# Kernel tuning notes

Measured on AMD Instinct MI355X. Metric: run time of the kernel, lower is better.

Reference implementation:

```python
import jax, jax.numpy as jnp
import numpy as np

EPS = 1e-5
C = 64  # in_channels == feat_channels == out_channels


def _ln(x, g, b):
    m = jnp.mean(x, axis=-1, keepdims=True)
    v = jnp.mean(jnp.square(x - m), axis=-1, keepdims=True)
    return (x - m) * jax.lax.rsqrt(v + EPS) * g + b


def setup_inputs() -> dict:
    key = jax.random.key(0)
    ks = jax.random.split(key, 10)
    bs, nc, H, W = 8, 80, 256, 256
    d = {
        "feat": jax.random.normal(ks[0], (bs, C, H, W), jnp.float32),
        "head": jax.random.normal(ks[1], (bs, nc, C, 1), jnp.float32),
        "pred": jax.random.normal(ks[2], (bs, nc, H // 2, W // 2), jnp.float32),
        # linear transforms (stored [in, out], applied as x @ W + b)
        "W_pred_t": jax.random.normal(ks[3], (C, 2 * C), jnp.float32) * 0.05,
        "b_pred_t": jnp.zeros((2 * C,), jnp.float32),
        "W_head_t": jax.random.normal(ks[4], (C, 2 * C), jnp.float32) * 0.05,
        "b_head_t": jnp.zeros((2 * C,), jnp.float32),
        "W_pred_g": jax.random.normal(ks[5], (C, C), jnp.float32) * 0.05,
        "b_pred_g": jnp.zeros((C,), jnp.float32),
        "W_head_g": jax.random.normal(ks[6], (C, C), jnp.float32) * 0.05,
        "b_head_g": jnp.zeros((C,), jnp.float32),
        "W_fc": jax.random.normal(ks[7], (C, C), jnp.float32) * 0.05,
        "b_fc": jnp.zeros((C,), jnp.float32),
        # layernorm params
        "g_pin": jnp.ones((C,), jnp.float32), "be_pin": jnp.zeros((C,), jnp.float32),
        "g_hin": jnp.ones((C,), jnp.float32), "be_hin": jnp.zeros((C,), jnp.float32),
        "g_pout": jnp.ones((C,), jnp.float32), "be_pout": jnp.zeros((C,), jnp.float32),
        "g_hout": jnp.ones((C,), jnp.float32), "be_hout": jnp.zeros((C,), jnp.float32),
        "g_fc": jnp.ones((C,), jnp.float32), "be_fc": jnp.zeros((C,), jnp.float32),
    }
    return d


def reference(feat, head, pred,
              W_pred_t, b_pred_t, W_head_t, b_head_t,
              W_pred_g, b_pred_g, W_head_g, b_head_g,
              W_fc, b_fc,
              g_pin, be_pin, g_hin, be_hin,
              g_pout, be_pout, g_hout, be_hout,
              g_fc, be_fc):
    bs, nc = head.shape[:2]
    H, W = feat.shape[2], feat.shape[3]
    pred_up = jax.image.resize(pred, (bs, nc, H, W), method="bilinear")
    pred_up = jax.nn.sigmoid(pred_up)
    # head-aware feature assembly: [bs, nc, C]
    assemble = jnp.einsum("bnhw,bchw->bnc", pred_up, feat)
    a = assemble.reshape(-1, C)                      # [BN, C]
    BN = a.shape[0]
    # head: [bs, nc, C, kk] -> [BN, kk, C]
    hd = jnp.transpose(head.reshape(bs, nc, C, -1), (0, 1, 3, 2)).reshape(BN, -1, C)

    pf = a @ W_pred_t + b_pred_t                     # [BN, 2C]
    pf_in, pf_out = pf[:, :C], pf[:, C:]
    hf = hd @ W_head_t + b_head_t                    # [BN, kk, 2C]
    hf_in, hf_out = hf[..., :C], hf[..., C:]

    gate = hf_in * pf_in[:, None, :]                 # [BN, kk, C]
    head_gate = jax.nn.sigmoid(_ln(gate @ W_head_g + b_head_g, g_hin, be_hin))
    pred_gate = jax.nn.sigmoid(_ln(gate @ W_pred_g + b_pred_g, g_pin, be_pin))

    hf_out = _ln(hf_out, g_hout, be_hout)
    pf_out = _ln(pf_out, g_pout, be_pout)

    upd = pred_gate * pf_out[:, None, :] + head_gate * hf_out
    upd = jax.nn.relu(_ln(upd @ W_fc + b_fc, g_fc, be_fc))
    upd = upd.reshape(bs, nc, -1, C)
    upd = jnp.transpose(upd, (0, 1, 3, 2)).reshape(bs, nc, C, 1, 1)
    return upd
```

## Files before the change

### kernel.cpp

```cpp
#include <hip/hip_runtime.h>
#include <hip/hip_bf16.h>


using bf16x8 = __attribute__((ext_vector_type(8))) short;
using f32x4  = __attribute__((ext_vector_type(4))) float;

#define NPART 64

__device__ __forceinline__ unsigned pk2(float lo, float hi) {
  union { __hip_bfloat162 h2; unsigned u; } cv;
  cv.h2 = __float22bfloat162_rn(make_float2(lo, hi));
  return cv.u;
}
__device__ __forceinline__ float sigAB(float a, float b) {
  return __builtin_amdgcn_rcpf(1.0f + __builtin_amdgcn_exp2f(-0.36067376f * a - 1.08202128f * b));
}
__device__ __forceinline__ float sigBA(float a, float b) {
  return __builtin_amdgcn_rcpf(1.0f + __builtin_amdgcn_exp2f(-1.08202128f * a - 0.36067376f * b));
}

__global__ __launch_bounds__(256, 2) void k_assemble(
    const float* __restrict__ feat, const float* __restrict__ pred,
    float* __restrict__ partial) {
  __shared__ __align__(16) unsigned short Pfrag[40 * 64 * 8];

  const int tid = threadIdx.x;
  const int b  = blockIdx.x >> 6;
  const int rb = blockIdx.x & 63;
  const int wid = tid >> 6, l = tid & 63;
  const int ch16 = l & 15, kg = l >> 4;
  const int c0 = wid << 4;
  const int h0 = rb * 4;
  const int gg = tid & 31, nb = tid >> 5;

  f32x4 acc[5] = {};

  const float* fwave = feat + (((size_t)(b * 64 + c0 + ch16)) << 16);
  const float* pbat  = pred + (((size_t)(b * 80)) << 14);

  float4 p0[10], p1[10];

  {
    const int j = h0 >> 1;
    const int r0 = (j > 0) ? j - 1 : 0, r1 = j;
    #pragma unroll
    for (int i = 0; i < 10; ++i) {
      const int n = nb + 8 * i;
      const float* pb = pbat + (((size_t)n) << 14);
      p0[i] = *(const float4*)(pb + (r0 << 7) + gg * 4);
      p1[i] = *(const float4*)(pb + (r1 << 7) + gg * 4);
    }
  }

  #pragma unroll
  for (int r = 0; r < 4; ++r) {
    const int h = h0 + r;
    const float wy0 = (r & 1) ? 0.75f : 0.25f;
    const float wy1 = (r & 1) ? 0.25f : 0.75f;

    #pragma unroll
    for (int i = 0; i < 10; ++i) {
      const int n = nb + 8 * i;
      const float y0 = wy0 * p0[i].x + wy1 * p1[i].x;
      const float y1 = wy0 * p0[i].y + wy1 * p1[i].y;
      const float y2 = wy0 * p0[i].z + wy1 * p1[i].z;
      const float y3 = wy0 * p0[i].w + wy1 * p1[i].w;
      float yl = __shfl_up(y3, 1, 64);   if (gg == 0)  yl = y0;
      float yr = __shfl_down(y0, 1, 64); if (gg == 31) yr = y3;
      float P[8];
      P[0] = sigAB(yl, y0); P[1] = sigBA(y0, y1);
      P[2] = sigAB(y0, y1); P[3] = sigBA(y1, y2);
      P[4] = sigAB(y1, y2); P[5] = sigBA(y2, y3);
      P[6] = sigAB(y2, y3); P[7] = sigBA(y3, yr);
      uint4 s;
      s.x = pk2(P[0], P[1]); s.y = pk2(P[2], P[3]);
      s.z = pk2(P[4], P[5]); s.w = pk2(P[6], P[7]);
      const int ks = gg >> 2, kgw = gg & 3;
      const int slot = kgw * 16 + ((n & 15) ^ ks);
      *(uint4*)&Pfrag[(((ks * 5 + (n >> 4)) * 64) + slot) * 8] = s;
    }
    __syncthreads();

    const float* fb = fwave + h * 256;
    float4 f[16];
    #pragma unroll
    for (int ks = 0; ks < 8; ++ks) {
      const int pw = ks * 32 + kg * 8;
      f[2 * ks]     = *(const float4*)(fb + pw);
      f[2 * ks + 1] = *(const float4*)(fb + pw + 4);
    }
    if (r < 3) {
      const int hn = h + 1;
      const int j = hn >> 1;
      int r0, r1;
      if ((hn & 1) == 0) { r0 = (j > 0) ? j - 1 : 0; r1 = j; }
      else               { r0 = j; r1 = (j < 127) ? j + 1 : 127; }
      #pragma unroll
      for (int i = 0; i < 10; ++i) {
        const int n = nb + 8 * i;
        const float* pb = pbat + (((size_t)n) << 14);
        p0[i] = *(const float4*)(pb + (r0 << 7) + gg * 4);
        p1[i] = *(const float4*)(pb + (r1 << 7) + gg * 4);
      }
    }
    #pragma unroll
    for (int ks = 0; ks < 8; ++ks) {
      const float4 f0 = f[2 * ks], f1 = f[2 * ks + 1];
      union { uint4 u; bf16x8 v; } bu;
      bu.u.x = pk2(f0.x, f0.y); bu.u.y = pk2(f0.z, f0.w);
      bu.u.z = pk2(f1.x, f1.y); bu.u.w = pk2(f1.z, f1.w);
      const int slot = kg * 16 + (ch16 ^ ks);
      #pragma unroll
      for (int m = 0; m < 5; ++m) {
        const bf16x8 af = *(const bf16x8*)&Pfrag[(((ks * 5 + m) * 64) + slot) * 8];
        acc[m] = __builtin_amdgcn_mfma_f32_16x16x32_bf16(af, bu.v, acc[m], 0, 0, 0);
      }
    }
    __syncthreads();
  }

  float* po = partial + ((size_t)(b * NPART + rb)) * (80 * 64);
  #pragma unroll
  for (int m = 0; m < 5; ++m) {
    #pragma unroll
    for (int q = 0; q < 4; ++q) {
      const int n = m * 16 + kg * 4 + q;
      po[n * 64 + c0 + ch16] = acc[m][q];
    }
  }
}

__device__ __forceinline__ float wred64(float v) {
  #pragma unroll
  for (int off = 32; off > 0; off >>= 1) v += __shfl_xor(v, off, 64);
  return v;
}
__device__ __forceinline__ float lnorm(float x, const float* __restrict__ g,
                                       const float* __restrict__ be, int l) {
  const float m = wred64(x) * 0.015625f;
  const float d = x - m;
  const float var = wred64(d * d) * 0.015625f;
  return d * rsqrtf(var + 1e-5f) * g[l] + be[l];
}
__device__ __forceinline__ float sigmf(float x) {
  return __builtin_amdgcn_rcpf(1.0f + __builtin_amdgcn_exp2f(-1.44269504f * x));
}

__global__ __launch_bounds__(256) void k_head(
    const float* __restrict__ partial, const float* __restrict__ head,
    const float* __restrict__ Wpt, const float* __restrict__ bpt,
    const float* __restrict__ Wht, const float* __restrict__ bht,
    const float* __restrict__ Wpg, const float* __restrict__ bpg,
    const float* __restrict__ Whg, const float* __restrict__ bhg,
    const float* __restrict__ Wfc, const float* __restrict__ bfc,
    const float* __restrict__ g_pin, const float* __restrict__ be_pin,
    const float* __restrict__ g_hin, const float* __restrict__ be_hin,
    const float* __restrict__ g_pout, const float* __restrict__ be_pout,
    const float* __restrict__ g_hout, const float* __restrict__ be_hout,
    const float* __restrict__ g_fc, const float* __restrict__ be_fc,
    float* __restrict__ out) {
  __shared__ float rows[4][4][64];
  const int tid = threadIdx.x, wid = tid >> 6, l = tid & 63;
  const int r = blockIdx.x * 4 + wid;
  const int b = r / 80, n = r % 80;

  const float* pp = partial + (size_t)b * (NPART * 80 * 64) + n * 64 + l;
  float a_c = 0.f;
  #pragma unroll 8
  for (int jj = 0; jj < NPART; ++jj) a_c += pp[(size_t)jj * (80 * 64)];
  rows[wid][0][l] = a_c;
  rows[wid][1][l] = head[(size_t)r * 64 + l];
  __syncthreads();

  float pf_in = bpt[l], pf_out = bpt[64 + l];
  float hf_in = bht[l], hf_out = bht[64 + l];
  #pragma unroll 8
  for (int c = 0; c < 64; ++c) {
    const float av = rows[wid][0][c];
    const float hv = rows[wid][1][c];
    pf_in  += av * Wpt[c * 128 + l];
    pf_out += av * Wpt[c * 128 + 64 + l];
    hf_in  += hv * Wht[c * 128 + l];
    hf_out += hv * Wht[c * 128 + 64 + l];
  }
  const float gate = hf_in * pf_in;
  rows[wid][2][l] = gate;
  __syncthreads();

  float hg = bhg[l], pg = bpg[l];
  #pragma unroll 8
  for (int c = 0; c < 64; ++c) {
    const float gv = rows[wid][2][c];
    hg += gv * Whg[c * 64 + l];
    pg += gv * Wpg[c * 64 + l];
  }
  const float head_gate = sigmf(lnorm(hg, g_hin, be_hin, l));
  const float pred_gate = sigmf(lnorm(pg, g_pin, be_pin, l));
  const float hfo = lnorm(hf_out, g_hout, be_hout, l);
  const float pfo = lnorm(pf_out, g_pout, be_pout, l);
  const float upd = pred_gate * pfo + head_gate * hfo;
  rows[wid][3][l] = upd;
  __syncthreads();

  float fc = bfc[l];
  #pragma unroll 8
  for (int c = 0; c < 64; ++c)
    fc += rows[wid][3][c] * Wfc[c * 64 + l];
  float o = lnorm(fc, g_fc, be_fc, l);
  o = fmaxf(o, 0.f);
  out[(size_t)r * 64 + l] = o;
}

extern "C" void kernel_launch(void* const* d_in, const int* in_sizes, int n_in,
                              void* d_out, int out_size, void* d_ws, size_t ws_size,
                              hipStream_t stream) {
  const float* feat   = (const float*)d_in[0];
  const float* head   = (const float*)d_in[1];
  const float* pred   = (const float*)d_in[2];
  const float* Wpt    = (const float*)d_in[3];
  const float* bpt    = (const float*)d_in[4];
  const float* Wht    = (const float*)d_in[5];
  const float* bht    = (const float*)d_in[6];
  const float* Wpg    = (const float*)d_in[7];
  const float* bpg    = (const float*)d_in[8];
  const float* Whg    = (const float*)d_in[9];
  const float* bhg    = (const float*)d_in[10];
  const float* Wfc    = (const float*)d_in[11];
  const float* bfc    = (const float*)d_in[12];
  const float* g_pin  = (const float*)d_in[13];
  const float* be_pin = (const float*)d_in[14];
  const float* g_hin  = (const float*)d_in[15];
  const float* be_hin = (const float*)d_in[16];
  const float* g_pout = (const float*)d_in[17];
  const float* be_pout= (const float*)d_in[18];
  const float* g_hout = (const float*)d_in[19];
  const float* be_hout= (const float*)d_in[20];
  const float* g_fc   = (const float*)d_in[21];
  const float* be_fc  = (const float*)d_in[22];
  float* out = (float*)d_out;
  float* partial = (float*)d_ws;

  hipLaunchKernelGGL(k_assemble, dim3(8 * NPART), dim3(256), 0, stream,
                     feat, pred, partial);
  hipLaunchKernelGGL(k_head, dim3(160), dim3(256), 0, stream,
                     partial, head, Wpt, bpt, Wht, bht, Wpg, bpg, Whg, bhg,
                     Wfc, bfc, g_pin, be_pin, g_hin, be_hin, g_pout, be_pout,
                     g_hout, be_hout, g_fc, be_fc, out);
}
```

Before: 64.28 us.

## Split assemble into more row blocks and parallelize head partial reduction

The assemble kernel is templated on rows per block. When the workspace is large enough it launches 1024 blocks of 2 rows instead of 512 blocks of 4, and the launch bound rises to 3 blocks per CU. The software prefetch of the next pred rows is removed: each iteration now loads its pred and feat rows up front, and __syncthreads is replaced by a raw LDS waitcnt plus s_barrier. The head kernel switches to one block per row, with four waves splitting the partial-sum reduction and a single wave doing the MLP. This aims for more parallelism and occupancy, at the cost of a larger partial buffer and lost load/compute overlap.

```diff
diff --git a/kernel.cpp b/kernel.cpp
--- a/kernel.cpp
+++ b/kernel.cpp
@@ -4,8 +4,6 @@
 
 using bf16x8 = __attribute__((ext_vector_type(8))) short;
 using f32x4  = __attribute__((ext_vector_type(4))) float;
-
-#define NPART 64
 
 __device__ __forceinline__ unsigned pk2(float lo, float hi) {
   union { __hip_bfloat162 h2; unsigned u; } cv;
@@ -19,52 +17,58 @@
   return __builtin_amdgcn_rcpf(1.0f + __builtin_amdgcn_exp2f(-1.08202128f * a - 0.36067376f * b));
 }
 
-__global__ __launch_bounds__(256, 2) void k_assemble(
+template<int ROWS>
+__global__ __launch_bounds__(256, 3) void k_assemble(
     const float* __restrict__ feat, const float* __restrict__ pred,
     float* __restrict__ partial) {
   __shared__ __align__(16) unsigned short Pfrag[40 * 64 * 8];
 
+  constexpr int LOGN = (ROWS == 2) ? 7 : 6;
   const int tid = threadIdx.x;
-  const int b  = blockIdx.x >> 6;
-  const int rb = blockIdx.x & 63;
+  const int b  = blockIdx.x >> LOGN;
+  const int rb = blockIdx.x & ((1 << LOGN) - 1);
   const int wid = tid >> 6, l = tid & 63;
   const int ch16 = l & 15, kg = l >> 4;
   const int c0 = wid << 4;
-  const int h0 = rb * 4;
+  const int h0 = rb * ROWS;
   const int gg = tid & 31, nb = tid >> 5;
 
   f32x4 acc[5] = {};
-
   const float* fwave = feat + (((size_t)(b * 64 + c0 + ch16)) << 16);
   const float* pbat  = pred + (((size_t)(b * 80)) << 14);
 
-  float4 p0[10], p1[10];
-
-  {
-    const int j = h0 >> 1;
-    const int r0 = (j > 0) ? j - 1 : 0, r1 = j;
+  #pragma unroll
+  for (int r = 0; r < ROWS; ++r) {
+    const int h = h0 + r;
+    const int j = h >> 1;
+    int r0, r1; float wy0, wy1;
+    if ((h & 1) == 0) { r0 = (j > 0) ? j - 1 : 0; r1 = j; wy0 = 0.25f; wy1 = 0.75f; }
+    else              { r0 = j; r1 = (j < 127) ? j + 1 : 127; wy0 = 0.75f; wy1 = 0.25f; }
+
+    float y[10][4];
     #pragma unroll
     for (int i = 0; i < 10; ++i) {
       const int n = nb + 8 * i;
       const float* pb = pbat + (((size_t)n) << 14);
-      p0[i] = *(const float4*)(pb + (r0 << 7) + gg * 4);
-      p1[i] = *(const float4*)(pb + (r1 << 7) + gg * 4);
-    }
-  }
-
-  #pragma unroll
-  for (int r = 0; r < 4; ++r) {
-    const int h = h0 + r;
-    const float wy0 = (r & 1) ? 0.75f : 0.25f;
-    const float wy1 = (r & 1) ? 0.25f : 0.75f;
+      const float4 v0 = *(const float4*)(pb + (r0 << 7) + gg * 4);
+      const float4 v1 = *(const float4*)(pb + (r1 << 7) + gg * 4);
+      y[i][0] = wy0 * v0.x + wy1 * v1.x; y[i][1] = wy0 * v0.y + wy1 * v1.y;
+      y[i][2] = wy0 * v0.z + wy1 * v1.z; y[i][3] = wy0 * v0.w + wy1 * v1.w;
+    }
+
+    const float* fb = fwave + h * 256;
+    float4 f[16];
+    #pragma unroll
+    for (int ks = 0; ks < 8; ++ks) {
+      const int pw = ks * 32 + kg * 8;
+      f[2 * ks]     = *(const float4*)(fb + pw);
+      f[2 * ks + 1] = *(const float4*)(fb + pw + 4);
+    }
 
     #pragma unroll
     for (int i = 0; i < 10; ++i) {
       const int n = nb + 8 * i;
-      const float y0 = wy0 * p0[i].x + wy1 * p1[i].x;
-      const float y1 = wy0 * p0[i].y + wy1 * p1[i].y;
-      const float y2 = wy0 * p0[i].z + wy1 * p1[i].z;
-      const float y3 = wy0 * p0[i].w + wy1 * p1[i].w;
+      const float y0 = y[i][0], y1 = y[i][1], y2 = y[i][2], y3 = y[i][3];
       float yl = __shfl_up(y3, 1, 64);   if (gg == 0)  yl = y0;
       float yr = __shfl_down(y0, 1, 64); if (gg == 31) yr = y3;
       float P[8];
@@ -79,30 +83,9 @@
       const int slot = kgw * 16 + ((n & 15) ^ ks);
       *(uint4*)&Pfrag[(((ks * 5 + (n >> 4)) * 64) + slot) * 8] = s;
     }
-    __syncthreads();
-
-    const float* fb = fwave + h * 256;
-    float4 f[16];
-    #pragma unroll
-    for (int ks = 0; ks < 8; ++ks) {
-      const int pw = ks * 32 + kg * 8;
-      f[2 * ks]     = *(const float4*)(fb + pw);
-      f[2 * ks + 1] = *(const float4*)(fb + pw + 4);
-    }
-    if (r < 3) {
-      const int hn = h + 1;
-      const int j = hn >> 1;
-      int r0, r1;
-      if ((hn & 1) == 0) { r0 = (j > 0) ? j - 1 : 0; r1 = j; }
-      else               { r0 = j; r1 = (j < 127) ? j + 1 : 127; }
-      #pragma unroll
-      for (int i = 0; i < 10; ++i) {
-        const int n = nb + 8 * i;
-        const float* pb = pbat + (((size_t)n) << 14);
-        p0[i] = *(const float4*)(pb + (r0 << 7) + gg * 4);
-        p1[i] = *(const float4*)(pb + (r1 << 7) + gg * 4);
-      }
-    }
+    asm volatile("s_waitcnt lgkmcnt(0)" ::: "memory");
+    __builtin_amdgcn_s_barrier();
+
     #pragma unroll
     for (int ks = 0; ks < 8; ++ks) {
       const float4 f0 = f[2 * ks], f1 = f[2 * ks + 1];
@@ -116,10 +99,11 @@
         acc[m] = __builtin_amdgcn_mfma_f32_16x16x32_bf16(af, bu.v, acc[m], 0, 0, 0);
       }
     }
-    __syncthreads();
+    asm volatile("s_waitcnt lgkmcnt(0)" ::: "memory");
+    __builtin_amdgcn_s_barrier();
   }
 
-  float* po = partial + ((size_t)(b * NPART + rb)) * (80 * 64);
+  float* po = partial + ((size_t)((b << LOGN) + rb)) * (80 * 64);
   #pragma unroll
   for (int m = 0; m < 5; ++m) {
     #pragma unroll
@@ -158,57 +142,59 @@
     const float* __restrict__ g_pout, const float* __restrict__ be_pout,
     const float* __restrict__ g_hout, const float* __restrict__ be_hout,
     const float* __restrict__ g_fc, const float* __restrict__ be_fc,
-    float* __restrict__ out) {
-  __shared__ float rows[4][4][64];
-  const int tid = threadIdx.x, wid = tid >> 6, l = tid & 63;
-  const int r = blockIdx.x * 4 + wid;
+    float* __restrict__ out, int npart) {
+  __shared__ float red[4][64];
+  __shared__ float buf[4][64];
+  const int tid = threadIdx.x, c = tid & 63, q = tid >> 6;
+  const int r = blockIdx.x;
   const int b = r / 80, n = r % 80;
-
-  const float* pp = partial + (size_t)b * (NPART * 80 * 64) + n * 64 + l;
-  float a_c = 0.f;
+  const int npq = npart >> 2;
+
+  const float* pp = partial + ((size_t)b * npart + (size_t)q * npq) * 5120 + n * 64 + c;
+  float s = 0.f;
   #pragma unroll 8
-  for (int jj = 0; jj < NPART; ++jj) a_c += pp[(size_t)jj * (80 * 64)];
-  rows[wid][0][l] = a_c;
-  rows[wid][1][l] = head[(size_t)r * 64 + l];
+  for (int jj = 0; jj < npq; ++jj) s += pp[(size_t)jj * 5120];
+  red[q][c] = s;
   __syncthreads();
 
-  float pf_in = bpt[l], pf_out = bpt[64 + l];
-  float hf_in = bht[l], hf_out = bht[64 + l];
-  #pragma unroll 8
-  for (int c = 0; c < 64; ++c) {
-    const float av = rows[wid][0][c];
-    const float hv = rows[wid][1][c];
-    pf_in  += av * Wpt[c * 128 + l];
-    pf_out += av * Wpt[c * 128 + 64 + l];
-    hf_in  += hv * Wht[c * 128 + l];
-    hf_out += hv * Wht[c * 128 + 64 + l];
+  if (q == 0) {
+    const float a_c = red[0][c] + red[1][c] + red[2][c] + red[3][c];
+    buf[0][c] = a_c;
+    buf[1][c] = head[(size_t)r * 64 + c];
+
+    float pf_in = bpt[c], pf_out = bpt[64 + c];
+    float hf_in = bht[c], hf_out = bht[64 + c];
+    #pragma unroll 8
+    for (int k = 0; k < 64; ++k) {
+      const float av = buf[0][k];
+      const float hv = buf[1][k];
+      pf_in  += av * Wpt[k * 128 + c];
+      pf_out += av * Wpt[k * 128 + 64 + c];
+      hf_in  += hv * Wht[k * 128 + c];
+      hf_out += hv * Wht[k * 128 + 64 + c];
+    }
+    buf[2][c] = hf_in * pf_in;
+
+    float hg = bhg[c], pg = bpg[c];
+    #pragma unroll 8
+    for (int k = 0; k < 64; ++k) {
+      const float gv = buf[2][k];
+      hg += gv * Whg[k * 64 + c];
+      pg += gv * Wpg[k * 64 + c];
+    }
+    const float head_gate = sigmf(lnorm(hg, g_hin, be_hin, c));
+    const float pred_gate = sigmf(lnorm(pg, g_pin, be_pin, c));
+    const float hfo = lnorm(hf_out, g_hout, be_hout, c);
+    const float pfo = lnorm(pf_out, g_pout, be_pout, c);
+    buf[3][c] = pred_gate * pfo + head_gate * hfo;
+
+    float fc = bfc[c];
+    #pragma unroll 8
+    for (int k = 0; k < 64; ++k)
+      fc += buf[3][k] * Wfc[k * 64 + c];
+    float o = lnorm(fc, g_fc, be_fc, c);
+    out[(size_t)r * 64 + c] = fmaxf(o, 0.f);
   }
-  const float gate = hf_in * pf_in;
-  rows[wid][2][l] = gate;
-  __syncthreads();
-
-  float hg = bhg[l], pg = bpg[l];
-  #pragma unroll 8
-  for (int c = 0; c < 64; ++c) {
-    const float gv = rows[wid][2][c];
-    hg += gv * Whg[c * 64 + l];
-    pg += gv * Wpg[c * 64 + l];
-  }
-  const float head_gate = sigmf(lnorm(hg, g_hin, be_hin, l));
-  const float pred_gate = sigmf(lnorm(pg, g_pin, be_pin, l));
-  const float hfo = lnorm(hf_out, g_hout, be_hout, l);
-  const float pfo = lnorm(pf_out, g_pout, be_pout, l);
-  const float upd = pred_gate * pfo + head_gate * hfo;
-  rows[wid][3][l] = upd;
-  __syncthreads();
-
-  float fc = bfc[l];
-  #pragma unroll 8
-  for (int c = 0; c < 64; ++c)
-    fc += rows[wid][3][c] * Wfc[c * 64 + l];
-  float o = lnorm(fc, g_fc, be_fc, l);
-  o = fmaxf(o, 0.f);
-  out[(size_t)r * 64 + l] = o;
 }
 
 extern "C" void kernel_launch(void* const* d_in, const int* in_sizes, int n_in,
@@ -240,10 +226,18 @@
   float* out = (float*)d_out;
   float* partial = (float*)d_ws;
 
-  hipLaunchKernelGGL(k_assemble, dim3(8 * NPART), dim3(256), 0, stream,
-                     feat, pred, partial);
-  hipLaunchKernelGGL(k_head, dim3(160), dim3(256), 0, stream,
+  const bool big = ws_size >= (size_t)8 * 128 * 5120 * 4;
+  const int npart = big ? 128 : 64;
+
+  if (big)
+    hipLaunchKernelGGL((k_assemble<2>), dim3(8 * 128), dim3(256), 0, stream,
+                       feat, pred, partial);
+  else
+    hipLaunchKernelGGL((k_assemble<4>), dim3(8 * 64), dim3(256), 0, stream,
+                       feat, pred, partial);
+
+  hipLaunchKernelGGL(k_head, dim3(640), dim3(256), 0, stream,
                      partial, head, Wpt, bpt, Wht, bht, Wpg, bpg, Whg, bhg,
                      Wfc, bfc, g_pin, be_pin, g_hin, be_hin, g_pout, be_pout,
-                     g_hout, be_hout, g_fc, be_fc, out);
-}
+                     g_hout, be_hout, g_fc, be_fc, out, npart);
+}
```

Measured after the change: 65.46 us. No clear change (+1.8%).
